# Kernel tuning notes

Hardware: AMD Instinct MI355X
Metric: run time of the kernel (lower is better)

Reference implementation:

```python
import jax, jax.numpy as jnp
import numpy as np

S, D = 4096, 2048  # seq_len, embedding_space == qkv_dim


def setup_inputs() -> dict:
    key = jax.random.key(0)
    k1, k2, k3, k4, k5 = jax.random.split(key, 5)
    return {
        "input_embedding": jax.random.normal(k1, (S, D), dtype=jnp.float32),
        "query_embedding": jax.random.normal(k2, (S, D), dtype=jnp.float32),
        "Wq": jax.random.normal(k3, (D, D), dtype=jnp.float32) * 0.02,
        "Wk": jax.random.normal(k4, (D, D), dtype=jnp.float32) * 0.02,
        "Wv": jax.random.normal(k5, (D, D), dtype=jnp.float32) * 0.02,
        "include_mask": 0,  # False -> causal mask applied (module's inverted logic)
    }


def reference(input_embedding, query_embedding, Wq, Wk, Wv, include_mask):
    q = query_embedding @ Wq          # [S, D]
    k = input_embedding @ Wk          # [S, D]
    v = input_embedding @ Wv          # [S, D]
    scores = (q @ k.T) / 10.0         # [S, S]; module hardcodes /10, not sqrt(d)
    if not include_mask:
        # causal: -inf strictly above the diagonal (triu with offset 1)
        s = scores.shape[0]
        causal = jnp.tril(jnp.ones((s, s), dtype=bool))
        scores = jnp.where(causal, scores, -jnp.inf)
    probs = jax.nn.softmax(scores, axis=-1)
    return probs @ v                  # [S, D]
```

## Files before the change

### kernel.cpp

```cpp
#include <hip/hip_runtime.h>
#include <hip/hip_bf16.h>
#include <math.h>

typedef __bf16 bf16_t;
typedef __bf16 bf16x8 __attribute__((ext_vector_type(8)));
typedef float f32x4 __attribute__((ext_vector_type(4)));

enum { EP_BF16 = 0, EP_SCORES = 1, EP_F32 = 2 };

#define MEMFENCE asm volatile("" ::: "memory")
#define BARRIER() do { MEMFENCE; __builtin_amdgcn_s_barrier(); MEMFENCE; } while (0)

__device__ __forceinline__ void gload_lds16(const void* g, void* l) {
  __builtin_amdgcn_global_load_lds(
      (const __attribute__((address_space(1))) void*)g,
      (__attribute__((address_space(3))) void*)l, 16, 0, 0);
}

__device__ __forceinline__ int xcd_swz(int bid, int nwg) {
  const int q = nwg >> 3;
  return (bid & 7) * q + (bid >> 3);
}


template <int TM, bool STG>
__device__ __forceinline__ void do_tile(char* smem, int slot, int sslot, size_t stoff,
                                        const char* const* gbase, const int* lbase,
                                        const int* aoff, const int* boff,
                                        f32x4 (&acc)[TM][4]) {
  bf16x8 bfr[4], af[4];
  if constexpr (TM == 8) {
#pragma unroll
    for (int n = 0; n < 4; ++n) bfr[n] = *(const bf16x8*)(smem + slot + boff[n]);
#pragma unroll
    for (int m = 0; m < 4; ++m) af[m] = *(const bf16x8*)(smem + slot + aoff[m]);
    if constexpr (STG) {
      gload_lds16(gbase[0] + stoff, smem + sslot + lbase[0]);
      gload_lds16(gbase[1] + stoff, smem + sslot + lbase[1]);
    }
    BARRIER();
    asm volatile("s_waitcnt lgkmcnt(0)" ::: "memory");
    __builtin_amdgcn_sched_barrier(0);
    __builtin_amdgcn_s_setprio(1);
#pragma unroll
    for (int m = 0; m < 4; ++m)
#pragma unroll
      for (int n = 0; n < 4; ++n)
        acc[m][n] = __builtin_amdgcn_mfma_f32_16x16x32_bf16(af[m], bfr[n], acc[m][n], 0, 0, 0);
    __builtin_amdgcn_s_setprio(0);
    BARRIER();
#pragma unroll
    for (int m = 0; m < 4; ++m) af[m] = *(const bf16x8*)(smem + slot + aoff[4 + m]);
    if constexpr (STG) {
      gload_lds16(gbase[2] + stoff, smem + sslot + lbase[2]);
      gload_lds16(gbase[3] + stoff, smem + sslot + lbase[3]);
      asm volatile("s_waitcnt vmcnt(8)" ::: "memory");
    }
    BARRIER();
    asm volatile("s_waitcnt lgkmcnt(0)" ::: "memory");
    __builtin_amdgcn_sched_barrier(0);
    __builtin_amdgcn_s_setprio(1);
#pragma unroll
    for (int m = 0; m < 4; ++m)
#pragma unroll
      for (int n = 0; n < 4; ++n)
        acc[4 + m][n] = __builtin_amdgcn_mfma_f32_16x16x32_bf16(af[m], bfr[n], acc[4 + m][n], 0, 0, 0);
    __builtin_amdgcn_s_setprio(0);
    BARRIER();
  } else {
#pragma unroll
    for (int n = 0; n < 4; ++n) bfr[n] = *(const bf16x8*)(smem + slot + boff[n]);
#pragma unroll
    for (int m = 0; m < 4; ++m) af[m] = *(const bf16x8*)(smem + slot + aoff[m]);
    if constexpr (STG) {
      gload_lds16(gbase[0] + stoff, smem + sslot + lbase[0]);
      gload_lds16(gbase[1] + stoff, smem + sslot + lbase[1]);
      gload_lds16(gbase[2] + stoff, smem + sslot + lbase[2]);
      asm volatile("s_waitcnt vmcnt(6)" ::: "memory");
    }
    BARRIER();
    asm volatile("s_waitcnt lgkmcnt(0)" ::: "memory");
    __builtin_amdgcn_sched_barrier(0);
    __builtin_amdgcn_s_setprio(1);
#pragma unroll
    for (int m = 0; m < 4; ++m)
#pragma unroll
      for (int n = 0; n < 4; ++n)
        acc[m][n] = __builtin_amdgcn_mfma_f32_16x16x32_bf16(af[m], bfr[n], acc[m][n], 0, 0, 0);
    __builtin_amdgcn_s_setprio(0);
    BARRIER();
  }
}

template <int TM, int EPI>
__device__ __forceinline__ void gemm_core(
    const bf16_t* __restrict__ A, const bf16_t* __restrict__ B,
    void* __restrict__ Cout, int M, int N, int K,
    int row0, int col0, bool causal, float scale, char* smem)
{
  constexpr int BM = TM * 32;
  constexpr int LPT_A = BM / 128;
  constexpr int LPT = LPT_A + 2;
  constexpr int ABYTES = BM * 64;
  constexpr int SLOT = (BM + 256) * 64;

  const int tid = threadIdx.x;
  const int w = tid >> 6, lane = tid & 63;
  const int wr = w >> 2, wc = w & 3;

  int Keff = K;
  if (EPI == EP_F32 && causal) Keff = min(K, row0 + BM);
  const int nt = Keff >> 5;

  const char* gbase[LPT];
  int lbase[LPT];
  {
    const int sd = (tid & 3) ^ ((tid >> 3) & 3);
    const int rrow = tid >> 2;
#pragma unroll
    for (int r = 0; r < LPT; ++r) {
      const bool isA = (r < LPT_A);
      const int rr = isA ? r : (r - LPT_A);
      const int grow = (isA ? row0 : col0) + rr * 128 + rrow;
      const bf16_t* op = isA ? A : B;
      gbase[r] = (const char*)(op + (size_t)grow * K) + sd * 16;
      lbase[r] = (isA ? 0 : ABYTES) + rr * 8192 + w * 1024;
    }
  }

  const int fl = lane & 15;
  const int arow_off = fl * 64 + (((lane >> 4) ^ ((fl >> 1) & 3)) * 16);
  int aoff[TM], boff[4];
#pragma unroll
  for (int m = 0; m < TM; ++m) aoff[m] = (wr * (TM * 16) + m * 16) * 64 + arow_off;
#pragma unroll
  for (int n = 0; n < 4; ++n) boff[n] = ABYTES + (wc * 64 + n * 16) * 64 + arow_off;

  f32x4 acc[TM][4] = {};

  const int npro = nt < 3 ? nt : 3;
  for (int t = 0; t < npro; ++t)
#pragma unroll
    for (int r = 0; r < LPT; ++r)
      gload_lds16(gbase[r] + (size_t)t * 64, smem + (t & 3) * SLOT + lbase[r]);

  const int nmain = nt - 3;
  if (nmain > 0) {
    if constexpr (TM == 8) asm volatile("s_waitcnt vmcnt(8)" ::: "memory");
    else                   asm volatile("s_waitcnt vmcnt(6)" ::: "memory");
    BARRIER();
    for (int t = 0; t < nmain; ++t)
      do_tile<TM, true>(smem, (t & 3) * SLOT, ((t + 3) & 3) * SLOT,
                        (size_t)(t + 3) * 64, gbase, lbase, aoff, boff, acc);
  }

  asm volatile("s_waitcnt vmcnt(0)" ::: "memory");
  BARRIER();
  for (int t = nmain > 0 ? nmain : 0; t < nt; ++t)
    do_tile<TM, false>(smem, (t & 3) * SLOT, 0, 0, gbase, lbase, aoff, boff, acc);

  const int cr = (lane >> 4) * 4;
  const int cc = lane & 15;
#pragma unroll
  for (int m = 0; m < TM; ++m) {
#pragma unroll
    for (int n = 0; n < 4; ++n) {
#pragma unroll
      for (int i = 0; i < 4; ++i) {
        const int r = row0 + wr * (TM * 16) + m * 16 + cr + i;
        const int c = col0 + wc * 64 + n * 16 + cc;
        float v = acc[m][n][i];
        if (EPI == EP_BF16) {
          ((bf16_t*)Cout)[(size_t)r * N + c] = (bf16_t)v;
        } else if (EPI == EP_SCORES) {
          v *= scale;
          if (causal && c > r) v = -INFINITY;
          ((float*)Cout)[(size_t)r * N + c] = v;
        } else {
          ((float*)Cout)[(size_t)r * N + c] = v;
        }
      }
    }
  }
}

__launch_bounds__(512, 2)
__global__ void qk_k(const bf16_t* __restrict__ qe16, const bf16_t* __restrict__ ie16,
                     const bf16_t* __restrict__ WqT, const bf16_t* __restrict__ WkT,
                     bf16_t* __restrict__ q16, bf16_t* __restrict__ k16) {
  extern __shared__ __align__(16) char smem[];
  int wg = xcd_swz(blockIdx.x, gridDim.x);
  const bf16_t *A, *B; bf16_t* C;
  if (wg < 128) { A = qe16; B = WqT; C = q16; }
  else          { A = ie16; B = WkT; C = k16; wg -= 128; }
  const int row0 = (wg >> 3) * 256, col0 = (wg & 7) * 256;
  gemm_core<8, EP_BF16>(A, B, C, 4096, 2048, 2048, row0, col0, false, 1.f, smem);
}

__launch_bounds__(512, 2)
__global__ void vs_k(const bf16_t* __restrict__ WvT, const bf16_t* __restrict__ ie16,
                     const bf16_t* __restrict__ q16, const bf16_t* __restrict__ k16,
                     bf16_t* __restrict__ vT16, float* __restrict__ scores,
                     const int* __restrict__ maskflag) {
  extern __shared__ __align__(16) char smem[];
  const bool causal = maskflag[0] == 0;
  const int bid = blockIdx.x;
  const int nsc = causal ? 136 : 256;
  if (bid < nsc) {
    const int sid = xcd_swz(bid, nsc);
    int r, c;
    if (causal) {
      r = (int)((sqrtf(8.f * (float)sid + 1.f) - 1.f) * 0.5f);
      while ((r + 1) * (r + 2) / 2 <= sid) ++r;
      while (r * (r + 1) / 2 > sid) --r;
      c = sid - r * (r + 1) / 2;
    } else {
      r = sid >> 4; c = sid & 15;
    }
    gemm_core<8, EP_SCORES>(q16, k16, scores, 4096, 4096, 2048,
                            r * 256, c * 256, causal, 0.1f, smem);
  } else {
    const int vloc = bid - nsc;
    if (vloc >= 256) return;
    const int wg = xcd_swz(vloc, 256);
    const int row0 = (wg >> 4) * 128, col0 = (wg & 15) * 256;
    gemm_core<4, EP_BF16>(WvT, ie16, vT16, 2048, 4096, 2048, row0, col0, false, 1.f, smem);
  }
}

template <int TM, int EPI>
__launch_bounds__(512, 2)
__global__ void gemm_k(const bf16_t* __restrict__ A, const bf16_t* __restrict__ B,
                       void* __restrict__ C, int M, int N, int K,
                       const int* __restrict__ maskflag, float scale) {
  extern __shared__ __align__(16) char smem[];
  const bool causal = (maskflag != nullptr) && (maskflag[0] == 0);
  constexpr int BM = TM * 32;
  const int ntn = N >> 8;
  const int wg = xcd_swz(blockIdx.x, gridDim.x);
  const int row0 = (wg / ntn) * BM, col0 = (wg % ntn) * 256;
  gemm_core<TM, EPI>(A, B, C, M, N, K, row0, col0, causal, scale, smem);
}


__global__ void cvt_k(const float* __restrict__ qe, const float* __restrict__ ie,
                      bf16_t* __restrict__ qe16, bf16_t* __restrict__ ie16, long n) {
  const float* x = blockIdx.y ? ie : qe;
  bf16_t* y = blockIdx.y ? ie16 : qe16;
  long i = ((long)blockIdx.x * blockDim.x + threadIdx.x) * 8;
  const long stride = (long)gridDim.x * blockDim.x * 8;
  for (; i < n; i += stride) {
    const float4 a = *(const float4*)(x + i);
    const float4 b = *(const float4*)(x + i + 4);
    bf16x8 o;
    o[0] = (__bf16)a.x; o[1] = (__bf16)a.y; o[2] = (__bf16)a.z; o[3] = (__bf16)a.w;
    o[4] = (__bf16)b.x; o[5] = (__bf16)b.y; o[6] = (__bf16)b.z; o[7] = (__bf16)b.w;
    *(bf16x8*)(y + i) = o;
  }
}

__global__ void trans_k(const float* __restrict__ Wq, const float* __restrict__ Wk,
                        const float* __restrict__ Wv,
                        bf16_t* __restrict__ WqT, bf16_t* __restrict__ WkT,
                        bf16_t* __restrict__ WvT, int Dm) {
  const float* W = blockIdx.z == 0 ? Wq : (blockIdx.z == 1 ? Wk : Wv);
  bf16_t* WT = blockIdx.z == 0 ? WqT : (blockIdx.z == 1 ? WkT : WvT);
  __shared__ float tile[32][33];
  const int bx = blockIdx.x, by = blockIdx.y;
  const int tx = threadIdx.x & 31, ty = threadIdx.x >> 5;
#pragma unroll
  for (int r = ty; r < 32; r += 8)
    tile[r][tx] = W[(size_t)(by * 32 + r) * Dm + bx * 32 + tx];
  __syncthreads();
#pragma unroll
  for (int r = ty; r < 32; r += 8)
    WT[(size_t)(bx * 32 + r) * Dm + by * 32 + tx] = (bf16_t)tile[tx][r];
}

__global__ void softmax_rows(const float* __restrict__ Sc, bf16_t* __restrict__ P,
                             int n, const int* __restrict__ maskflag) {
  const int row = blockIdx.x;
  const int tid = threadIdx.x;
  const bool causal = maskflag[0] == 0;
  const int L = causal ? (row + 1) : n;
  const float* srow = Sc + (size_t)row * n;
  float v[16];
  float m = -INFINITY;
#pragma unroll
  for (int j = 0; j < 16; ++j) {
    const int idx = tid + j * 256;
    v[j] = (idx < L) ? srow[idx] : -INFINITY;
    m = fmaxf(m, v[j]);
  }
#pragma unroll
  for (int off = 32; off >= 1; off >>= 1) m = fmaxf(m, __shfl_xor(m, off));
  __shared__ float redm[4];
  __shared__ float reds[4];
  if ((tid & 63) == 0) redm[tid >> 6] = m;
  __syncthreads();
  m = fmaxf(fmaxf(redm[0], redm[1]), fmaxf(redm[2], redm[3]));
  float s = 0.f;
#pragma unroll
  for (int j = 0; j < 16; ++j) {
    v[j] = __expf(v[j] - m);
    s += v[j];
  }
#pragma unroll
  for (int off = 32; off >= 1; off >>= 1) s += __shfl_xor(s, off);
  if ((tid & 63) == 0) reds[tid >> 6] = s;
  __syncthreads();
  s = reds[0] + reds[1] + reds[2] + reds[3];
  const float inv = 1.f / s;
  bf16_t* prow = P + (size_t)row * n;
#pragma unroll
  for (int j = 0; j < 16; ++j) prow[tid + j * 256] = (bf16_t)(v[j] * inv);
}

extern "C" void kernel_launch(void* const* d_in, const int* in_sizes, int n_in,
                              void* d_out, int out_size, void* d_ws, size_t ws_size,
                              hipStream_t stream) {
  const float* ie = (const float*)d_in[0];
  const float* qe = (const float*)d_in[1];
  const float* Wq = (const float*)d_in[2];
  const float* Wk = (const float*)d_in[3];
  const float* Wv = (const float*)d_in[4];
  const int* mask = (const int*)d_in[5];
  float* out = (float*)d_out;

  const int S = 4096, D = 2048;
  char* ws = (char*)d_ws;
  const size_t MB = 1u << 20;
  bf16_t* q16  = (bf16_t*)(ws + 0 * MB);
  bf16_t* k16  = (bf16_t*)(ws + 16 * MB);
  bf16_t* vT16 = (bf16_t*)(ws + 32 * MB);
  bf16_t* ie16 = (bf16_t*)(ws + 48 * MB);
  bf16_t* WvT  = (bf16_t*)(ws + 64 * MB);
  bf16_t* qe16 = (bf16_t*)(ws + 72 * MB);
  bf16_t* WqT  = (bf16_t*)(ws + 88 * MB);
  bf16_t* WkT  = (bf16_t*)(ws + 96 * MB);
  float*  scores = (float*)(ws + 72 * MB);
  bf16_t* probs  = (bf16_t*)(ws + 0 * MB);

  hipFuncSetAttribute(reinterpret_cast<const void*>(&qk_k),
                      hipFuncAttributeMaxDynamicSharedMemorySize, 131072);
  hipFuncSetAttribute(reinterpret_cast<const void*>(&vs_k),
                      hipFuncAttributeMaxDynamicSharedMemorySize, 131072);
  hipFuncSetAttribute(reinterpret_cast<const void*>(&gemm_k<4, EP_F32>),
                      hipFuncAttributeMaxDynamicSharedMemorySize, 98304);

  cvt_k<<<dim3(1024, 2), 256, 0, stream>>>(qe, ie, qe16, ie16, (long)S * D);
  trans_k<<<dim3(D / 32, D / 32, 3), 256, 0, stream>>>(Wq, Wk, Wv, WqT, WkT, WvT, D);

  qk_k<<<256, 512, 131072, stream>>>(qe16, ie16, WqT, WkT, q16, k16);

  vs_k<<<512, 512, 131072, stream>>>(WvT, ie16, q16, k16, vT16, scores, mask);

  softmax_rows<<<S, 256, 0, stream>>>(scores, probs, S, mask);

  gemm_k<4, EP_F32><<<256, 512, 98304, stream>>>(probs, vT16, out, S, D, S, mask, 1.f);
}
```

Baseline: 275.3 us.

## Rebalance V projection across kernels and split-K the causal PV GEMM with atomics

The V-projection tiles are now split between the scores kernel and the softmax kernel. Under the causal mask, the scores kernel fills its idle slots with the first 120 V tiles and the softmax kernel computes the remaining 136 alongside two-rows-per-block softmax. The final P·V GEMM becomes a load-balanced split-K. The longest causal bands are split in two and accumulated with float atomics into an output that the conversion kernel zeroes beforehand. The aim is to remove load imbalance from the causal triangle and the separate softmax launch. The cost is atomic traffic, an extra zeroing pass, and non-deterministic summation order.

```diff
diff --git a/kernel.cpp b/kernel.cpp
--- a/kernel.cpp
+++ b/kernel.cpp
@@ -6,7 +6,7 @@
 typedef __bf16 bf16x8 __attribute__((ext_vector_type(8)));
 typedef float f32x4 __attribute__((ext_vector_type(4)));
 
-enum { EP_BF16 = 0, EP_SCORES = 1, EP_F32 = 2 };
+enum { EP_BF16 = 0, EP_SCORES = 1, EP_F32 = 2, EP_F32A = 3 };
 
 #define MEMFENCE asm volatile("" ::: "memory")
 #define BARRIER() do { MEMFENCE; __builtin_amdgcn_s_barrier(); MEMFENCE; } while (0)
@@ -95,7 +95,7 @@
 template <int TM, int EPI>
 __device__ __forceinline__ void gemm_core(
     const bf16_t* __restrict__ A, const bf16_t* __restrict__ B,
-    void* __restrict__ Cout, int M, int N, int K,
+    void* __restrict__ Cout, int Nout, int kstride, int klen,
     int row0, int col0, bool causal, float scale, char* smem)
 {
   constexpr int BM = TM * 32;
@@ -108,9 +108,7 @@
   const int w = tid >> 6, lane = tid & 63;
   const int wr = w >> 2, wc = w & 3;
 
-  int Keff = K;
-  if (EPI == EP_F32 && causal) Keff = min(K, row0 + BM);
-  const int nt = Keff >> 5;
+  const int nt = klen >> 5;
 
   const char* gbase[LPT];
   int lbase[LPT];
@@ -123,7 +121,7 @@
       const int rr = isA ? r : (r - LPT_A);
       const int grow = (isA ? row0 : col0) + rr * 128 + rrow;
       const bf16_t* op = isA ? A : B;
-      gbase[r] = (const char*)(op + (size_t)grow * K) + sd * 16;
+      gbase[r] = (const char*)(op + (size_t)grow * kstride) + sd * 16;
       lbase[r] = (isA ? 0 : ABYTES) + rr * 8192 + w * 1024;
     }
   }
@@ -171,13 +169,15 @@
         const int c = col0 + wc * 64 + n * 16 + cc;
         float v = acc[m][n][i];
         if (EPI == EP_BF16) {
-          ((bf16_t*)Cout)[(size_t)r * N + c] = (bf16_t)v;
+          ((bf16_t*)Cout)[(size_t)r * Nout + c] = (bf16_t)v;
         } else if (EPI == EP_SCORES) {
           v *= scale;
           if (causal && c > r) v = -INFINITY;
-          ((float*)Cout)[(size_t)r * N + c] = v;
+          ((float*)Cout)[(size_t)r * Nout + c] = v;
+        } else if (EPI == EP_F32) {
+          ((float*)Cout)[(size_t)r * Nout + c] = v;
         } else {
-          ((float*)Cout)[(size_t)r * N + c] = v;
+          atomicAdd((float*)Cout + (size_t)r * Nout + c, v);
         }
       }
     }
@@ -194,7 +194,7 @@
   if (wg < 128) { A = qe16; B = WqT; C = q16; }
   else          { A = ie16; B = WkT; C = k16; wg -= 128; }
   const int row0 = (wg >> 3) * 256, col0 = (wg & 7) * 256;
-  gemm_core<8, EP_BF16>(A, B, C, 4096, 2048, 2048, row0, col0, false, 1.f, smem);
+  gemm_core<8, EP_BF16>(A, B, C, 2048, 2048, 2048, row0, col0, false, 1.f, smem);
 }
 
 __launch_bounds__(512, 2)
@@ -204,8 +204,8 @@
                      const int* __restrict__ maskflag) {
   extern __shared__ __align__(16) char smem[];
   const bool causal = maskflag[0] == 0;
+  const int nsc = causal ? 136 : 256;
   const int bid = blockIdx.x;
-  const int nsc = causal ? 136 : 256;
   if (bid < nsc) {
     const int sid = xcd_swz(bid, nsc);
     int r, c;
@@ -217,45 +217,128 @@
     } else {
       r = sid >> 4; c = sid & 15;
     }
-    gemm_core<8, EP_SCORES>(q16, k16, scores, 4096, 4096, 2048,
+    gemm_core<8, EP_SCORES>(q16, k16, scores, 4096, 2048, 2048,
                             r * 256, c * 256, causal, 0.1f, smem);
   } else {
-    const int vloc = bid - nsc;
-    if (vloc >= 256) return;
-    const int wg = xcd_swz(vloc, 256);
-    const int row0 = (wg >> 4) * 128, col0 = (wg & 15) * 256;
-    gemm_core<4, EP_BF16>(WvT, ie16, vT16, 2048, 4096, 2048, row0, col0, false, 1.f, smem);
-  }
-}
-
-template <int TM, int EPI>
+    const int j = bid - nsc;
+    gemm_core<4, EP_BF16>(WvT, ie16, vT16, 4096, 2048, 2048,
+                          (j >> 4) * 128, (j & 15) * 256, false, 1.f, smem);
+  }
+}
+
 __launch_bounds__(512, 2)
-__global__ void gemm_k(const bf16_t* __restrict__ A, const bf16_t* __restrict__ B,
-                       void* __restrict__ C, int M, int N, int K,
-                       const int* __restrict__ maskflag, float scale) {
+__global__ void smv_k(const bf16_t* __restrict__ WvT, const bf16_t* __restrict__ ie16,
+                      bf16_t* __restrict__ vT16,
+                      const float* __restrict__ scores, bf16_t* __restrict__ probs,
+                      const int* __restrict__ maskflag) {
   extern __shared__ __align__(16) char smem[];
-  const bool causal = (maskflag != nullptr) && (maskflag[0] == 0);
-  constexpr int BM = TM * 32;
-  const int ntn = N >> 8;
-  const int wg = xcd_swz(blockIdx.x, gridDim.x);
-  const int row0 = (wg / ntn) * BM, col0 = (wg % ntn) * 256;
-  gemm_core<TM, EPI>(A, B, C, M, N, K, row0, col0, causal, scale, smem);
+  const bool causal = maskflag[0] == 0;
+  const int nv = causal ? 136 : 256;
+  const int vbase = causal ? 120 : 0;
+  const int bid = blockIdx.x;
+  if (bid < nv) {
+    const int j = vbase + bid;
+    gemm_core<4, EP_BF16>(WvT, ie16, vT16, 4096, 2048, 2048,
+                          (j >> 4) * 128, (j & 15) * 256, false, 1.f, smem);
+    return;
+  }
+  const int p = bid - nv;
+  if (p >= 2048) return;
+  const int tid = threadIdx.x;
+  const int h = tid >> 8;
+  const int t = tid & 255;
+  const int row = 2 * p + h;
+  const int L = causal ? (row + 1) : 4096;
+  const float* srow = scores + (size_t)row * 4096;
+  float v[16];
+  float m = -INFINITY;
+#pragma unroll
+  for (int j = 0; j < 16; ++j) {
+    const int idx = t + j * 256;
+    v[j] = (idx < L) ? srow[idx] : -INFINITY;
+    m = fmaxf(m, v[j]);
+  }
+#pragma unroll
+  for (int off = 32; off >= 1; off >>= 1) m = fmaxf(m, __shfl_xor(m, off));
+  __shared__ float redm[8];
+  __shared__ float reds[8];
+  if ((tid & 63) == 0) redm[tid >> 6] = m;
+  __syncthreads();
+  m = fmaxf(fmaxf(redm[4 * h + 0], redm[4 * h + 1]),
+            fmaxf(redm[4 * h + 2], redm[4 * h + 3]));
+  float s = 0.f;
+#pragma unroll
+  for (int j = 0; j < 16; ++j) {
+    v[j] = __expf(v[j] - m);
+    s += v[j];
+  }
+#pragma unroll
+  for (int off = 32; off >= 1; off >>= 1) s += __shfl_xor(s, off);
+  if ((tid & 63) == 0) reds[tid >> 6] = s;
+  __syncthreads();
+  s = reds[4 * h + 0] + reds[4 * h + 1] + reds[4 * h + 2] + reds[4 * h + 3];
+  const float inv = 1.f / s;
+  bf16_t* prow = probs + (size_t)row * 4096;
+#pragma unroll
+  for (int j = 0; j < 16; ++j) prow[t + j * 256] = (bf16_t)(v[j] * inv);
+}
+
+__launch_bounds__(512, 2)
+__global__ void pv_k(const bf16_t* __restrict__ probs, const bf16_t* __restrict__ vT16,
+                     float* __restrict__ out, const int* __restrict__ maskflag) {
+  extern __shared__ __align__(16) char smem[];
+  const bool causal = maskflag[0] == 0;
+  const int bid = blockIdx.x;
+  int band, col, k0, klen; bool at;
+  if (causal) {
+    if (bid < 256) {
+      const int t = bid >> 1;
+      band = 16 + (t >> 3); col = t & 7;
+      const int Keff = 128 * (band + 1);
+      klen = Keff >> 1; k0 = (bid & 1) ? klen : 0; at = true;
+    } else if (bid < 384) {
+      const int t = bid - 256;
+      band = t >> 3; col = t & 7;
+      k0 = 0; klen = 128 * (band + 1); at = false;
+    } else return;
+  } else {
+    if (bid >= 512) return;
+    const int t = bid >> 1;
+    band = t >> 3; col = t & 7;
+    klen = 2048; k0 = (bid & 1) ? 2048 : 0; at = true;
+  }
+  if (at)
+    gemm_core<4, EP_F32A>(probs + k0, vT16 + k0, out, 2048, 4096, klen,
+                          band * 128, col * 256, false, 1.f, smem);
+  else
+    gemm_core<4, EP_F32>(probs + k0, vT16 + k0, out, 2048, 4096, klen,
+                         band * 128, col * 256, false, 1.f, smem);
 }
 
 
 __global__ void cvt_k(const float* __restrict__ qe, const float* __restrict__ ie,
-                      bf16_t* __restrict__ qe16, bf16_t* __restrict__ ie16, long n) {
-  const float* x = blockIdx.y ? ie : qe;
-  bf16_t* y = blockIdx.y ? ie16 : qe16;
+                      bf16_t* __restrict__ qe16, bf16_t* __restrict__ ie16,
+                      float* __restrict__ zout, long n) {
+  const int y = blockIdx.y;
   long i = ((long)blockIdx.x * blockDim.x + threadIdx.x) * 8;
   const long stride = (long)gridDim.x * blockDim.x * 8;
+  if (y == 2) {
+    const float4 z = make_float4(0.f, 0.f, 0.f, 0.f);
+    for (; i < n; i += stride) {
+      *(float4*)(zout + i) = z;
+      *(float4*)(zout + i + 4) = z;
+    }
+    return;
+  }
+  const float* x = y ? ie : qe;
+  bf16_t* o = y ? ie16 : qe16;
   for (; i < n; i += stride) {
     const float4 a = *(const float4*)(x + i);
     const float4 b = *(const float4*)(x + i + 4);
-    bf16x8 o;
-    o[0] = (__bf16)a.x; o[1] = (__bf16)a.y; o[2] = (__bf16)a.z; o[3] = (__bf16)a.w;
-    o[4] = (__bf16)b.x; o[5] = (__bf16)b.y; o[6] = (__bf16)b.z; o[7] = (__bf16)b.w;
-    *(bf16x8*)(y + i) = o;
+    bf16x8 u;
+    u[0] = (__bf16)a.x; u[1] = (__bf16)a.y; u[2] = (__bf16)a.z; u[3] = (__bf16)a.w;
+    u[4] = (__bf16)b.x; u[5] = (__bf16)b.y; u[6] = (__bf16)b.z; u[7] = (__bf16)b.w;
+    *(bf16x8*)(o + i) = u;
   }
 }
 
@@ -275,45 +358,6 @@
 #pragma unroll
   for (int r = ty; r < 32; r += 8)
     WT[(size_t)(bx * 32 + r) * Dm + by * 32 + tx] = (bf16_t)tile[tx][r];
-}
-
-__global__ void softmax_rows(const float* __restrict__ Sc, bf16_t* __restrict__ P,
-                             int n, const int* __restrict__ maskflag) {
-  const int row = blockIdx.x;
-  const int tid = threadIdx.x;
-  const bool causal = maskflag[0] == 0;
-  const int L = causal ? (row + 1) : n;
-  const float* srow = Sc + (size_t)row * n;
-  float v[16];
-  float m = -INFINITY;
-#pragma unroll
-  for (int j = 0; j < 16; ++j) {
-    const int idx = tid + j * 256;
-    v[j] = (idx < L) ? srow[idx] : -INFINITY;
-    m = fmaxf(m, v[j]);
-  }
-#pragma unroll
-  for (int off = 32; off >= 1; off >>= 1) m = fmaxf(m, __shfl_xor(m, off));
-  __shared__ float redm[4];
-  __shared__ float reds[4];
-  if ((tid & 63) == 0) redm[tid >> 6] = m;
-  __syncthreads();
-  m = fmaxf(fmaxf(redm[0], redm[1]), fmaxf(redm[2], redm[3]));
-  float s = 0.f;
-#pragma unroll
-  for (int j = 0; j < 16; ++j) {
-    v[j] = __expf(v[j] - m);
-    s += v[j];
-  }
-#pragma unroll
-  for (int off = 32; off >= 1; off >>= 1) s += __shfl_xor(s, off);
-  if ((tid & 63) == 0) reds[tid >> 6] = s;
-  __syncthreads();
-  s = reds[0] + reds[1] + reds[2] + reds[3];
-  const float inv = 1.f / s;
-  bf16_t* prow = P + (size_t)row * n;
-#pragma unroll
-  for (int j = 0; j < 16; ++j) prow[tid + j * 256] = (bf16_t)(v[j] * inv);
 }
 
 extern "C" void kernel_launch(void* const* d_in, const int* in_sizes, int n_in,
@@ -345,17 +389,19 @@
                       hipFuncAttributeMaxDynamicSharedMemorySize, 131072);
   hipFuncSetAttribute(reinterpret_cast<const void*>(&vs_k),
                       hipFuncAttributeMaxDynamicSharedMemorySize, 131072);
-  hipFuncSetAttribute(reinterpret_cast<const void*>(&gemm_k<4, EP_F32>),
+  hipFuncSetAttribute(reinterpret_cast<const void*>(&smv_k),
                       hipFuncAttributeMaxDynamicSharedMemorySize, 98304);
-
-  cvt_k<<<dim3(1024, 2), 256, 0, stream>>>(qe, ie, qe16, ie16, (long)S * D);
+  hipFuncSetAttribute(reinterpret_cast<const void*>(&pv_k),
+                      hipFuncAttributeMaxDynamicSharedMemorySize, 98304);
+
+  cvt_k<<<dim3(1024, 3), 256, 0, stream>>>(qe, ie, qe16, ie16, out, (long)S * D);
   trans_k<<<dim3(D / 32, D / 32, 3), 256, 0, stream>>>(Wq, Wk, Wv, WqT, WkT, WvT, D);
 
   qk_k<<<256, 512, 131072, stream>>>(qe16, ie16, WqT, WkT, q16, k16);
 
-  vs_k<<<512, 512, 131072, stream>>>(WvT, ie16, q16, k16, vT16, scores, mask);
-
-  softmax_rows<<<S, 256, 0, stream>>>(scores, probs, S, mask);
-
-  gemm_k<4, EP_F32><<<256, 512, 98304, stream>>>(probs, vT16, out, S, D, S, mask, 1.f);
-}
+  vs_k<<<256, 512, 131072, stream>>>(WvT, ie16, q16, k16, vT16, scores, mask);
+
+  smv_k<<<2304, 512, 98304, stream>>>(WvT, ie16, vT16, scores, probs, mask);
+
+  pv_k<<<512, 512, 98304, stream>>>(probs, vT16, out, mask);
+}
```

After: 282.5 us. 2.6% more time.
